# Performance work log

Measured on AMD Instinct MI355X. Metric: run time of the kernel, lower is better.

Reference implementation:

```python
import jax, jax.numpy as jnp
import numpy as np

PI = np.float32(np.pi)

def _sinc_tf_style(x):
    # Faithful to the TF code: replace x==0 by 1.0 BEFORE sin(pi*x)/(pi*x).
    x = jnp.where(x == 0, jnp.float32(1.0), x)
    pix = PI * x
    return jnp.sin(pix) / pix

def setup_inputs() -> dict:
    key = jax.random.key(0)
    k1, k2 = jax.random.split(key)
    B, H, W, C = 2, 256, 256, 2
    img = jax.random.normal(k1, (B, H, W, C), dtype=jnp.float32)
    fmap = jax.random.normal(k2, (B, H, W, C), dtype=jnp.float32)  # flow along H
    return {"img": img, "fmap": fmap}

def reference(img, fmap):
    # img, fmap: [B, H, W, C]; 1D sinc-kernel warp along axis 1 (H).
    B, H, W, C = img.shape
    j = jnp.arange(H, dtype=jnp.float32)
    # source coordinate for each input row i: i_x[b,i,w,c] = clip(f + i, 0, H-1)
    i_x = jnp.clip(fmap + j[None, :, None, None], 0.0, jnp.float32(H - 1))
    # Kf[b,i,j,w,c] = sinc(i_x[b,i,w,c] - j)   -> [B, H, H, W, C]
    diff = i_x[:, :, None, :, :] - j[None, None, :, None, None]
    Kf = _sinc_tf_style(diff)
    # out[b,j,w,c] = sum_i img[b,i,w,c] * Kf[b,i,j,w,c]
    out = jnp.einsum('biwc,bijwc->bjwc', img, Kf)
    return out
```

## Files before the change

### kernel.cpp

```cpp
#include <hip/hip_runtime.h>
#include <cmath>

constexpr int Bn = 2, Hn = 256, Wn = 256, Cn = 2;
constexpr int NG = 8;
constexpr int NJ = 2;

__global__ __launch_bounds__(512, 8) void sinc_main_kernel(
    const float* __restrict__ img, const float* __restrict__ fmap,
    float* __restrict__ out)
{
    const float INV_PI = 0x1.45f306p-2f;

    __shared__ __align__(16) float sh_x[Cn][Hn];
    __shared__ __align__(16) float sh_p[Cn][Hn];
    __shared__ float sh_acc[NG][128 * Cn];

    const int bid = blockIdx.x;
    const int b   = bid >> 9;
    const int w   = (bid >> 1) & 255;
    const int jh  = bid & 1;
    const int t   = threadIdx.x;
    const int wv  = t >> 6;
    const int l   = t & 63;

    {
        const int i = 32 * wv + (l >> 1), c = l & 1;
        const size_t off = (((size_t)b * Hn + i) * Wn + w) * Cn + c;
        const float f = fmap[off];
        float x0 = fminf(fmaxf(f + (float)i, 0.0f), 255.0f);
        const float n = rintf(x0);
        const float r = x0 - n;
        float sp = __builtin_amdgcn_sinf(0.5f * r) * INV_PI;
        if (((int)n) & 1) sp = -sp;
        const float p = img[off] * sp;
        if (p == 0.0f) x0 += 0x1p-15f;
        sh_x[c][i] = x0;
        sh_p[c][i] = p;
    }
    __asm__ volatile("s_waitcnt lgkmcnt(0)" ::: "memory");

    const int jl = l;

    float acc[NJ][2];
#pragma unroll
    for (int jj = 0; jj < NJ; ++jj) { acc[jj][0] = 0.0f; acc[jj][1] = 0.0f; }

    const float4* qx = (const float4*)sh_x;
    const float4* qp = (const float4*)sh_p;

#pragma unroll 2
    for (int qd = 0; qd < 8; ++qd) {
        const int iq = wv * 8 + qd;
        const float4 x0q = qx[iq],      p0q = qp[iq];
        const float4 x1q = qx[64 + iq], p1q = qp[64 + iq];
#pragma unroll
        for (int jj = 0; jj < NJ; ++jj) {
            const float J = (float)(128 * jh + jl + 64 * jj);
            {
                const float d0 = x0q.x - J, d1 = x0q.y - J;
                const float d2 = x0q.z - J, d3 = x0q.w - J;
                const float m01 = d0 * d1, m23 = d2 * d3;
                const float n01 = fmaf(p0q.x, d1, p0q.y * d0);
                const float n23 = fmaf(p0q.z, d3, p0q.w * d2);
                const float Nv  = fmaf(n01, m23, n23 * m01);
                acc[jj][0] = fmaf(Nv, __builtin_amdgcn_rcpf(m01 * m23), acc[jj][0]);
            }
            {
                const float d0 = x1q.x - J, d1 = x1q.y - J;
                const float d2 = x1q.z - J, d3 = x1q.w - J;
                const float m01 = d0 * d1, m23 = d2 * d3;
                const float n01 = fmaf(p1q.x, d1, p1q.y * d0);
                const float n23 = fmaf(p1q.z, d3, p1q.w * d2);
                const float Nv  = fmaf(n01, m23, n23 * m01);
                acc[jj][1] = fmaf(Nv, __builtin_amdgcn_rcpf(m01 * m23), acc[jj][1]);
            }
        }
    }

#pragma unroll
    for (int jj = 0; jj < NJ; ++jj) {
        const int lj = jl + 64 * jj;
        *(float2*)&sh_acc[wv][lj * 2] = make_float2(acc[jj][0], acc[jj][1]);
    }
    __syncthreads();

    if (t < 128) {
        float a0 = 0.0f, a1 = 0.0f;
#pragma unroll
        for (int g = 0; g < NG; ++g) {
            const float2 v = *(const float2*)&sh_acc[g][t * 2];
            a0 += v.x; a1 += v.y;
        }
        const int j = 128 * jh + t;
        const float sgn = (j & 1) ? -1.0f : 1.0f;
        float2* o = (float2*)&out[(((size_t)b * Hn + j) * Wn + w) * Cn];
        *o = make_float2(sgn * a0, sgn * a1);
    }
}

extern "C" void kernel_launch(void* const* d_in, const int* in_sizes, int n_in,
                              void* d_out, int out_size, void* d_ws, size_t ws_size,
                              hipStream_t stream)
{
    (void)in_sizes; (void)n_in; (void)out_size; (void)d_ws; (void)ws_size;
    const float* img  = (const float*)d_in[0];
    const float* fmap = (const float*)d_in[1];
    float* out = (float*)d_out;
    sinc_main_kernel<<<Bn * Wn * 2, 512, 0, stream>>>(img, fmap, out);
}
```

Baseline: 13.29 us.

## Split each column over four 256-thread blocks with one output row per thread

Launches four blocks per (batch, column) instead of two, each with four waves covering 64 output rows. Each thread now computes one output row over 64 input rows instead of two rows over 32. It also loops over two input rows in the prologue. This aims for smaller blocks, a shorter reduction and better scheduling, but the shared-memory loads are no longer reused across two outputs and the sin prologue is repeated by more blocks.

```diff
diff --git a/kernel.cpp b/kernel.cpp
--- a/kernel.cpp
+++ b/kernel.cpp
@@ -2,10 +2,9 @@
 #include <cmath>
 
 constexpr int Bn = 2, Hn = 256, Wn = 256, Cn = 2;
-constexpr int NG = 8;
-constexpr int NJ = 2;
+constexpr int NW = 4;
 
-__global__ __launch_bounds__(512, 8) void sinc_main_kernel(
+__global__ __launch_bounds__(256, 8) void sinc_main_kernel(
     const float* __restrict__ img, const float* __restrict__ fmap,
     float* __restrict__ out)
 {
@@ -13,18 +12,19 @@
 
     __shared__ __align__(16) float sh_x[Cn][Hn];
     __shared__ __align__(16) float sh_p[Cn][Hn];
-    __shared__ float sh_acc[NG][128 * Cn];
+    __shared__ float sh_acc[NW][64 * Cn];
 
     const int bid = blockIdx.x;
-    const int b   = bid >> 9;
-    const int w   = (bid >> 1) & 255;
-    const int jh  = bid & 1;
+    const int b   = bid >> 10;
+    const int w   = (bid >> 2) & 255;
+    const int jq  = bid & 3;
     const int t   = threadIdx.x;
     const int wv  = t >> 6;
     const int l   = t & 63;
 
-    {
-        const int i = 32 * wv + (l >> 1), c = l & 1;
+#pragma unroll
+    for (int k = 0; k < 2; ++k) {
+        const int i = 64 * wv + 32 * k + (l >> 1), c = l & 1;
         const size_t off = (((size_t)b * Hn + i) * Wn + w) * Cn + c;
         const float f = fmap[off];
         float x0 = fminf(fmaxf(f + (float)i, 0.0f), 255.0f);
@@ -39,59 +39,49 @@
     }
     __asm__ volatile("s_waitcnt lgkmcnt(0)" ::: "memory");
 
-    const int jl = l;
+    const float J = (float)(64 * jq + l);
 
-    float acc[NJ][2];
-#pragma unroll
-    for (int jj = 0; jj < NJ; ++jj) { acc[jj][0] = 0.0f; acc[jj][1] = 0.0f; }
+    float acc0 = 0.0f, acc1 = 0.0f;
 
     const float4* qx = (const float4*)sh_x;
     const float4* qp = (const float4*)sh_p;
 
-#pragma unroll 2
-    for (int qd = 0; qd < 8; ++qd) {
-        const int iq = wv * 8 + qd;
+#pragma unroll 1
+    for (int qd = 0; qd < 16; ++qd) {
+        const int iq = wv * 16 + qd;
         const float4 x0q = qx[iq],      p0q = qp[iq];
         const float4 x1q = qx[64 + iq], p1q = qp[64 + iq];
-#pragma unroll
-        for (int jj = 0; jj < NJ; ++jj) {
-            const float J = (float)(128 * jh + jl + 64 * jj);
-            {
-                const float d0 = x0q.x - J, d1 = x0q.y - J;
-                const float d2 = x0q.z - J, d3 = x0q.w - J;
-                const float m01 = d0 * d1, m23 = d2 * d3;
-                const float n01 = fmaf(p0q.x, d1, p0q.y * d0);
-                const float n23 = fmaf(p0q.z, d3, p0q.w * d2);
-                const float Nv  = fmaf(n01, m23, n23 * m01);
-                acc[jj][0] = fmaf(Nv, __builtin_amdgcn_rcpf(m01 * m23), acc[jj][0]);
-            }
-            {
-                const float d0 = x1q.x - J, d1 = x1q.y - J;
-                const float d2 = x1q.z - J, d3 = x1q.w - J;
-                const float m01 = d0 * d1, m23 = d2 * d3;
-                const float n01 = fmaf(p1q.x, d1, p1q.y * d0);
-                const float n23 = fmaf(p1q.z, d3, p1q.w * d2);
-                const float Nv  = fmaf(n01, m23, n23 * m01);
-                acc[jj][1] = fmaf(Nv, __builtin_amdgcn_rcpf(m01 * m23), acc[jj][1]);
-            }
+        {
+            const float d0 = x0q.x - J, d1 = x0q.y - J;
+            const float d2 = x0q.z - J, d3 = x0q.w - J;
+            const float m01 = d0 * d1, m23 = d2 * d3;
+            const float n01 = fmaf(p0q.x, d1, p0q.y * d0);
+            const float n23 = fmaf(p0q.z, d3, p0q.w * d2);
+            const float Nv  = fmaf(n01, m23, n23 * m01);
+            acc0 = fmaf(Nv, __builtin_amdgcn_rcpf(m01 * m23), acc0);
+        }
+        {
+            const float d0 = x1q.x - J, d1 = x1q.y - J;
+            const float d2 = x1q.z - J, d3 = x1q.w - J;
+            const float m01 = d0 * d1, m23 = d2 * d3;
+            const float n01 = fmaf(p1q.x, d1, p1q.y * d0);
+            const float n23 = fmaf(p1q.z, d3, p1q.w * d2);
+            const float Nv  = fmaf(n01, m23, n23 * m01);
+            acc1 = fmaf(Nv, __builtin_amdgcn_rcpf(m01 * m23), acc1);
         }
     }
 
-#pragma unroll
-    for (int jj = 0; jj < NJ; ++jj) {
-        const int lj = jl + 64 * jj;
-        *(float2*)&sh_acc[wv][lj * 2] = make_float2(acc[jj][0], acc[jj][1]);
-    }
+    *(float2*)&sh_acc[wv][l * 2] = make_float2(acc0, acc1);
     __syncthreads();
 
-    if (t < 128) {
+    if (t < 64) {
         float a0 = 0.0f, a1 = 0.0f;
 #pragma unroll
-        for (int g = 0; g < NG; ++g) {
+        for (int g = 0; g < NW; ++g) {
             const float2 v = *(const float2*)&sh_acc[g][t * 2];
             a0 += v.x; a1 += v.y;
         }
-        const int j = 128 * jh + t;
+        const int j = 64 * jq + t;
         const float sgn = (j & 1) ? -1.0f : 1.0f;
         float2* o = (float2*)&out[(((size_t)b * Hn + j) * Wn + w) * Cn];
         *o = make_float2(sgn * a0, sgn * a1);
@@ -106,5 +96,5 @@
     const float* img  = (const float*)d_in[0];
     const float* fmap = (const float*)d_in[1];
     float* out = (float*)d_out;
-    sinc_main_kernel<<<Bn * Wn * 2, 512, 0, stream>>>(img, fmap, out);
+    sinc_main_kernel<<<Bn * Wn * 4, 256, 0, stream>>>(img, fmap, out);
 }
```

New measurement: 14.80 us. 11.4% more time.
